# Performance work log

Hardware: AMD Instinct MI355X
Metric: run time of the kernel (lower is better)

Reference implementation:

```python
import jax, jax.numpy as jnp
import numpy as np
import math

HEADS = 8
DIM_HEAD = 64

def setup_inputs() -> dict:
    key = jax.random.key(0)
    ks = jax.random.split(key, 6)
    B, L, D = 2, 2048, 512
    Ls = 1936
    inner = HEADS * DIM_HEAD  # 512
    x = jax.random.normal(ks[0], (B, L, D), dtype=jnp.float32)
    positions = jax.random.normal(ks[1], (B, Ls, 2), dtype=jnp.float32) * 10.0
    w_qkv = jax.random.normal(ks[2], (3 * inner, D), dtype=jnp.float32) * (1.0 / math.sqrt(D))
    w_out = jax.random.normal(ks[3], (D, inner), dtype=jnp.float32) * (1.0 / math.sqrt(inner))
    b_out = jnp.zeros((D,), dtype=jnp.float32)
    log_sigma = jnp.full((HEADS,), math.log(3.0), dtype=jnp.float32)
    global_bias = jnp.float32(0.0)
    return {"x": x, "positions": positions, "w_qkv": w_qkv, "w_out": w_out,
            "b_out": b_out, "log_sigma": log_sigma, "global_bias": global_bias,
            "num_spatial": Ls}

def reference(x, positions, w_qkv, w_out, b_out, log_sigma, global_bias, num_spatial):
    B, L, D = x.shape
    H, Dh = HEADS, DIM_HEAD
    scale = Dh ** (-0.5)
    # qkv projection: [B,L,3*H*Dh] -> q,k,v each [B,H,L,Dh]
    qkv = jnp.einsum('bld,ed->ble', x, w_qkv)
    q, k, v = jnp.split(qkv, 3, axis=-1)
    def heads(t):
        return t.reshape(B, L, H, Dh).transpose(0, 2, 1, 3)
    q, k, v = heads(q), heads(k), heads(v)
    attn = jnp.einsum('bhid,bhjd->bhij', q, k) * scale  # [B,H,L,L]
    # Gaussian distance bias on the spatial block, global_bias elsewhere
    Ls = num_spatial
    diff = positions[:, :, None, :] - positions[:, None, :, :]  # [B,Ls,Ls,2]
    dist_sq = jnp.sum(diff * diff, axis=-1)                     # [B,Ls,Ls]
    sigma_sq = jnp.exp(log_sigma) ** 2                          # [H]
    spatial_bias = -dist_sq[:, None] / (2.0 * sigma_sq[None, :, None, None])  # [B,H,Ls,Ls]
    full_bias = jnp.full((B, H, L, L), global_bias, dtype=x.dtype)
    full_bias = full_bias.at[:, :, :Ls, :Ls].set(spatial_bias)
    attn = jax.nn.softmax(attn + full_bias, axis=-1)
    out = jnp.einsum('bhij,bhjd->bhid', attn, v)  # [B,H,L,Dh]
    out = out.transpose(0, 2, 1, 3).reshape(B, L, H * Dh)
    return jnp.einsum('ble,de->bld', out, w_out) + b_out
```

## Files before the change

kernel.cpp:

```cpp
#include <hip/hip_runtime.h>
#include <stdint.h>
#include <stddef.h>

#define NB   2
#define NL   2048
#define ND   512
#define NH   8
#define DH   64
#define LOG2E 1.44269504f
#define RG_TOT 32768
#define JS   4

typedef __attribute__((ext_vector_type(8))) short bf16x8;
typedef __attribute__((ext_vector_type(4))) float f32x4;

__device__ __forceinline__ unsigned short f2bf(float f) {
  union { float f; unsigned int u; } c; c.f = f;
  unsigned int u = c.u;
  unsigned int r = u + 0x7fffu + ((u >> 16) & 1u);
  return (unsigned short)(r >> 16);
}

__device__ __forceinline__ float bf2f(unsigned short u) {
  union { unsigned int i; float f; } c; c.i = ((unsigned int)u) << 16; return c.f;
}

__device__ __forceinline__ void split2(float v, unsigned short& h, unsigned short& l) {
  h = f2bf(v);
  l = f2bf(v - bf2f(h));
}

__device__ __forceinline__ float fexp2(float x) {
#if __has_builtin(__builtin_amdgcn_exp2f)
  return __builtin_amdgcn_exp2f(x);
#else
  return exp2f(x);
#endif
}

__device__ __forceinline__ void gl_lds16(const unsigned short* g, unsigned short* l) {
#if __has_builtin(__builtin_amdgcn_global_load_lds)
  __builtin_amdgcn_global_load_lds(
      (const __attribute__((address_space(1))) unsigned int*)g,
      (__attribute__((address_space(3))) unsigned int*)l, 16, 0, 0);
#else
  *(uint4*)l = *(const uint4*)g;
#endif
}

#define XC  524288
#define WQC 196608
#define WOC 65536
#define TOTC (XC + WQC + WOC)
__global__ void cvt_f32_bf16(const float* __restrict__ x, const float* __restrict__ wq,
                             const float* __restrict__ wo, const float* __restrict__ positions,
                             const int* __restrict__ ns_p,
                             unsigned short* __restrict__ xb, unsigned short* __restrict__ wqb,
                             unsigned short* __restrict__ wob, float* __restrict__ pospad) {
  int idx = blockIdx.x * 256 + threadIdx.x;
  if (idx < TOTC) {
    const float* src; unsigned short* dst; int off;
    if (idx < XC)            { src = x;  dst = xb;  off = idx; }
    else if (idx < XC + WQC) { src = wq; dst = wqb; off = idx - XC; }
    else                     { src = wo; dst = wob; off = idx - XC - WQC; }
    float4 f = ((const float4*)src)[off];
    ushort4 o;
    o.x = f2bf(f.x); o.y = f2bf(f.y); o.z = f2bf(f.z); o.w = f2bf(f.w);
    ((ushort4*)dst)[off] = o;
  } else {
    int i2 = idx - TOTC;
    if (i2 < NB * 1024) {
      int b = i2 >> 10;
      int jj = (i2 & 1023) * 2;
      int Ls = ns_p[0];
      float4 o = make_float4(0.f, 0.f, 0.f, 0.f);
      if (jj < Ls) { o.x = positions[((size_t)b * Ls + jj) * 2];
                     o.y = positions[((size_t)b * Ls + jj) * 2 + 1]; }
      if (jj + 1 < Ls) { o.z = positions[((size_t)b * Ls + jj + 1) * 2];
                         o.w = positions[((size_t)b * Ls + jj + 1) * 2 + 1]; }
      *(float4*)&pospad[((size_t)b * NL + jj) * 2] = o;
    }
  }
}

__global__ __launch_bounds__(256, 2) void gemm_qkv(
    const unsigned short* __restrict__ A, const unsigned short* __restrict__ Bm,
    unsigned short* __restrict__ qo, unsigned short* __restrict__ kp,
    unsigned short* __restrict__ vo)
{
  __shared__ __align__(16) unsigned short S[128 * 32 + 128 * 32];
  const int tid = threadIdx.x, wid = tid >> 6, lane = tid & 63;
  const int quad = lane >> 4, l15 = lane & 15;
  const int m0 = blockIdx.x * 128, n0 = blockIdx.y * 128;
  const int wm = (wid >> 1) * 64, wn = (wid & 1) * 64;

  f32x4 acc[4][4];
#pragma unroll
  for (int a = 0; a < 4; ++a)
#pragma unroll
    for (int b = 0; b < 4; ++b)
#pragma unroll
      for (int z = 0; z < 4; ++z) acc[a][b][z] = 0.f;

  for (int k0 = 0; k0 < ND; k0 += 32) {
#pragma unroll
    for (int p = 0; p < 4; ++p) {
      int c = p * 256 + wid * 64 + lane;
      if (c < 512) {
        int row = c >> 2, off = c & 3;
        gl_lds16(A + (size_t)(m0 + row) * ND + k0 + off * 8, &S[c * 8]);
      } else {
        int cb = c - 512;
        int row = cb >> 2, off = cb & 3;
        gl_lds16(Bm + (size_t)(n0 + row) * ND + k0 + off * 8, &S[c * 8]);
      }
    }
    __syncthreads();
    bf16x8 af[4], bfr[4];
#pragma unroll
    for (int mb = 0; mb < 4; ++mb)
      af[mb] = *(const bf16x8*)&S[(wm + mb * 16 + l15) * 32 + quad * 8];
#pragma unroll
    for (int nb = 0; nb < 4; ++nb)
      bfr[nb] = *(const bf16x8*)&S[4096 + (wn + nb * 16 + l15) * 32 + quad * 8];
#pragma unroll
    for (int mb = 0; mb < 4; ++mb)
#pragma unroll
      for (int nb = 0; nb < 4; ++nb)
        acc[mb][nb] = __builtin_amdgcn_mfma_f32_16x16x32_bf16(af[mb], bfr[nb], acc[mb][nb], 0, 0, 0);
    __syncthreads();
  }

  const float QSCALE = 0.125f * LOG2E;
#pragma unroll
  for (int mb = 0; mb < 4; ++mb) {
    int e0 = m0 + wm + mb * 16 + quad * 4;
    int s   = e0 >> 9;
    int hh  = (e0 >> 6) & 7;
    if (s == 1) {
      int kc  = mb >> 1;
      int q_t = ((mb & 1) << 1) + (quad >> 1);
      int par = quad & 1;
#pragma unroll
      for (int nb = 0; nb < 4; ++nb) {
        int token = n0 + wn + nb * 16 + l15;
        int bb = token >> 11, ll = token & 2047;
        int jt = ll >> 4;
        ushort4 o;
        o.x = f2bf(acc[mb][nb][0]);
        o.y = f2bf(acc[mb][nb][1]);
        o.z = f2bf(acc[mb][nb][2]);
        o.w = f2bf(acc[mb][nb][3]);
        size_t addr = (((size_t)(bb * NH + hh) * 128 + jt) * 2 + kc) * 512
                    + (q_t * 16 + l15) * 8 + par * 4;
        *(ushort4*)&kp[addr] = o;
      }
    } else {
      unsigned short* dst = (s == 0) ? qo : vo;
      float sc = (s == 0) ? QSCALE : 1.0f;
      int dh0 = e0 & 63;
#pragma unroll
      for (int nb = 0; nb < 4; ++nb) {
        int token = n0 + wn + nb * 16 + l15;
        int bb = token >> 11, ll = token & 2047;
        ushort4 o;
        o.x = f2bf(acc[mb][nb][0] * sc);
        o.y = f2bf(acc[mb][nb][1] * sc);
        o.z = f2bf(acc[mb][nb][2] * sc);
        o.w = f2bf(acc[mb][nb][3] * sc);
        *(ushort4*)&dst[(((size_t)bb * NH + hh) * NL + ll) * DH + dh0] = o;
      }
    }
  }
}

__global__ __launch_bounds__(256) void repack_v(
    const unsigned short* __restrict__ v, unsigned short* __restrict__ vp,
    const float* __restrict__ pospad, const float* __restrict__ log_sigma,
    const float* __restrict__ gbias_p, const int* __restrict__ ns_p,
    unsigned short* __restrict__ kext, unsigned short* __restrict__ qext)
{
  __shared__ unsigned short T[64][74];
  const int l0 = blockIdx.x * 64;
  const int bh = blockIdx.y;
  const int b  = bh >> 3, h = bh & 7;
  const int Ls = ns_p[0];
  const float gb  = gbias_p[0];
  const float sig = __expf(log_sigma[h]);
  const float CI  = LOG2E * 0.5f / (sig * sig);
  const float LGB = LOG2E * gb;
  const float* posb = pospad + (size_t)b * NL * 2;
  const int tid = threadIdx.x;

  const unsigned short* src = v + ((size_t)bh * NL + l0) * DH;
  unsigned short* dst = vp + (size_t)bh * 131072 + (size_t)(l0 >> 5) * 2048;
#pragma unroll
  for (int p = 0; p < 2; ++p) {
    int c = p * 256 + tid;
    int row = c >> 3, seg = c & 7;
    *(uint4*)&T[row][seg * 8] = *(const uint4*)(src + row * DH + seg * 8);
  }
  __syncthreads();
#pragma unroll
  for (int p = 0; p < 2; ++p) {
    int c = p * 256 + tid;
    int l15 = c & 15, q = (c >> 4) & 3, dht = (c >> 6) & 3, jcl = c >> 8;
    unsigned short u[8];
#pragma unroll
    for (int t = 0; t < 8; ++t) u[t] = T[jcl * 32 + q * 8 + t][dht * 16 + l15];
    *(uint4*)(dst + (size_t)jcl * 2048 + dht * 512 + (q * 16 + l15) * 8) = *(uint4*)u;
  }

  {
    int jtl  = tid >> 6;
    int lane = tid & 63;
    int quad = lane >> 4, l15 = lane & 15;
    int j = l0 + jtl * 16 + l15;
    unsigned short bv[16];
#pragma unroll
    for (int z = 0; z < 16; ++z) bv[z] = 0;
    if (j < Ls) {
      float2 p2 = *(const float2*)(posb + (size_t)j * 2);
      float rjC = -(CI * (p2.x * p2.x + p2.y * p2.y));
      unsigned short one = f2bf(1.0f);
      bv[0] = one; bv[1] = one;
      split2(rjC, bv[2], bv[3]);
      unsigned short Xh, Xl, Yh, Yl;
      split2(2.0f * CI * p2.x, Xh, Xl);
      split2(2.0f * CI * p2.y, Yh, Yl);
      bv[4] = Xh; bv[5] = Xh; bv[6] = Xl;
      bv[7] = Yh; bv[8] = Yh; bv[9] = Yl;
    }
    unsigned short o[8];
#pragma unroll
    for (int z = 0; z < 8; ++z) o[z] = bv[quad * 8 + z < 16 ? quad * 8 + z : 15];
    if (quad >= 2) {
#pragma unroll
      for (int z = 0; z < 8; ++z) o[z] = 0;
    }
    *(uint4*)(kext + ((size_t)bh * 128 + (l0 >> 4) + jtl) * 512 + lane * 8) = *(uint4*)o;
  }

  {
    int row = tid >> 2, seg = tid & 3;
    int i = l0 + row;
    unsigned short av[16];
#pragma unroll
    for (int z = 0; z < 16; ++z) av[z] = 0;
    if (i < Ls) {
      float2 p2 = *(const float2*)(posb + (size_t)i * 2);
      float riCm = -(CI * (p2.x * p2.x + p2.y * p2.y)) - LGB;
      unsigned short one = f2bf(1.0f);
      split2(riCm, av[0], av[1]);
      av[2] = one; av[3] = one;
      unsigned short xh, xl, yh, yl;
      split2(p2.x, xh, xl);
      split2(p2.y, yh, yl);
      av[4] = xh; av[5] = xl; av[6] = xh;
      av[7] = yh; av[8] = yl; av[9] = yh;
    }
    unsigned short o[8];
#pragma unroll
    for (int z = 0; z < 8; ++z) o[z] = (seg * 8 + z < 16) ? av[seg * 8 + z] : 0;
    if (seg >= 2) {
#pragma unroll
      for (int z = 0; z < 8; ++z) o[z] = 0;
    }
    *(uint4*)(qext + ((size_t)bh * NL + i) * 32 + seg * 8) = *(uint4*)o;
  }
}

__global__ __launch_bounds__(256, 2) void flash_kernel(
    const unsigned short* __restrict__ qb, const unsigned short* __restrict__ qeb,
    const unsigned short* __restrict__ kp, const unsigned short* __restrict__ keb,
    const unsigned short* __restrict__ vp, const float* __restrict__ gbias_p,
    unsigned short* __restrict__ Pb, float* __restrict__ rsbuf)
{
  const int it = blockIdx.x >> 2;
  const int js = blockIdx.x & 3;
  const int h  = blockIdx.y;
  const int b  = blockIdx.z;
  const int i0 = it * 128;
  const int jbase = js * (NL / JS);
  const float CBL = -8.0f * LOG2E + LOG2E * gbias_p[0];

  const int tid  = threadIdx.x;
  const int wid  = tid >> 6;
  const int lane = tid & 63;
  const int quad = lane >> 4;
  const int l15  = lane & 15;

  __shared__ __align__(16) unsigned short Ps[128][78];

  const size_t bh = (size_t)b * NH + h;
  const unsigned short* qbase  = qb  + (bh * NL + i0 + wid * 32) * DH;
  const unsigned short* qebase = qeb + (bh * NL + i0 + wid * 32) * 32;
  const unsigned short* kpb    = kp  + bh * 131072;
  const unsigned short* kebb   = keb + bh * 65536;
  const unsigned short* vpb    = vp  + bh * 131072;

  bf16x8 qf[2][2], qfe[2];
#pragma unroll
  for (int ib = 0; ib < 2; ++ib) {
#pragma unroll
    for (int kc = 0; kc < 2; ++kc)
      qf[ib][kc] = *(const bf16x8*)(qbase + (size_t)(ib * 16 + l15) * DH + kc * 32 + quad * 8);
    qfe[ib] = *(const bf16x8*)(qebase + (size_t)(ib * 16 + l15) * 32 + quad * 8);
  }

  f32x4 accO[4][2];
  float rsum[2];
#pragma unroll
  for (int d = 0; d < 4; ++d)
#pragma unroll
    for (int ib = 0; ib < 2; ++ib)
#pragma unroll
      for (int z = 0; z < 4; ++z) accO[d][ib][z] = 0.f;
  rsum[0] = 0.f; rsum[1] = 0.f;

  for (int jt = 0; jt < NL / JS / 64; ++jt) {
    const int j0 = jbase + jt * 64;
    const int jt0 = j0 >> 4;

    bf16x8 vf[4][2];
#pragma unroll
    for (int dht = 0; dht < 4; ++dht)
#pragma unroll
      for (int jc = 0; jc < 2; ++jc)
        vf[dht][jc] = *(const bf16x8*)(vpb + ((size_t)((j0 >> 5) + jc) * 4 + dht) * 512 + lane * 8);

#pragma unroll
    for (int jb = 0; jb < 4; ++jb) {
      bf16x8 kf0 = *(const bf16x8*)(kpb + ((size_t)(jt0 + jb) * 2 + 0) * 512 + lane * 8);
      bf16x8 kf1 = *(const bf16x8*)(kpb + ((size_t)(jt0 + jb) * 2 + 1) * 512 + lane * 8);
      bf16x8 kfe = *(const bf16x8*)(kebb + (size_t)(jt0 + jb) * 512 + lane * 8);
#pragma unroll
      for (int ib = 0; ib < 2; ++ib) {
        f32x4 accS;
#pragma unroll
        for (int z = 0; z < 4; ++z) accS[z] = 0.f;
        accS = __builtin_amdgcn_mfma_f32_16x16x32_bf16(kf0, qf[ib][0], accS, 0, 0, 0);
        accS = __builtin_amdgcn_mfma_f32_16x16x32_bf16(kf1, qf[ib][1], accS, 0, 0, 0);
        accS = __builtin_amdgcn_mfma_f32_16x16x32_bf16(kfe, qfe[ib], accS, 0, 0, 0);
        float p0 = fexp2(accS[0] + CBL);
        float p1 = fexp2(accS[1] + CBL);
        float p2 = fexp2(accS[2] + CBL);
        float p3 = fexp2(accS[3] + CBL);
        rsum[ib] += (p0 + p1) + (p2 + p3);
        uint2 w;
        w.x = (uint32_t)f2bf(p0) | ((uint32_t)f2bf(p1) << 16);
        w.y = (uint32_t)f2bf(p2) | ((uint32_t)f2bf(p3) << 16);
        *(uint2*)&Ps[wid * 32 + ib * 16 + l15][jb * 16 + quad * 4] = w;
      }
    }

    bf16x8 pf[2][2];
#pragma unroll
    for (int ib = 0; ib < 2; ++ib)
#pragma unroll
      for (int jc = 0; jc < 2; ++jc)
        pf[ib][jc] = *(const bf16x8*)&Ps[wid * 32 + ib * 16 + l15][jc * 32 + quad * 8];
#pragma unroll
    for (int dht = 0; dht < 4; ++dht)
#pragma unroll
      for (int ib = 0; ib < 2; ++ib) {
        accO[dht][ib] = __builtin_amdgcn_mfma_f32_16x16x32_bf16(vf[dht][0], pf[ib][0], accO[dht][ib], 0, 0, 0);
        accO[dht][ib] = __builtin_amdgcn_mfma_f32_16x16x32_bf16(vf[dht][1], pf[ib][1], accO[dht][ib], 0, 0, 0);
      }
  }

  const size_t rgbase = bh * NL + i0;
  const size_t poff = (size_t)js * RG_TOT * DH;
#pragma unroll
  for (int ib = 0; ib < 2; ++ib) {
    float v = rsum[ib];
    v += __shfl_xor(v, 16);
    v += __shfl_xor(v, 32);
    int irow = wid * 32 + ib * 16 + l15;
    if (quad == 0)
      rsbuf[(size_t)js * RG_TOT + rgbase + irow] = v;
#pragma unroll
    for (int dht = 0; dht < 4; ++dht) {
      ushort4 o;
      o.x = f2bf(accO[dht][ib][0]);
      o.y = f2bf(accO[dht][ib][1]);
      o.z = f2bf(accO[dht][ib][2]);
      o.w = f2bf(accO[dht][ib][3]);
      *(ushort4*)&Pb[poff + (rgbase + irow) * DH + dht * 16 + quad * 4] = o;
    }
  }
}

__global__ __launch_bounds__(256) void combine_kernel(const unsigned short* __restrict__ Pb,
                                                      const float* __restrict__ rsbuf,
                                                      unsigned short* __restrict__ attnb) {
  int idx = blockIdx.x * 256 + threadIdx.x;
  int rg = idx >> 4, c4 = idx & 15;
  float s0 = 0.f, s1 = 0.f, s2 = 0.f, s3 = 0.f, rsum = 0.f;
#pragma unroll
  for (int js = 0; js < JS; ++js) {
    ushort4 u = *(const ushort4*)&Pb[((size_t)js * RG_TOT + rg) * DH + c4 * 4];
    s0 += bf2f(u.x); s1 += bf2f(u.y); s2 += bf2f(u.z); s3 += bf2f(u.w);
    rsum += rsbuf[(size_t)js * RG_TOT + rg];
  }
  float rs = 1.0f / rsum;
  int bhm = rg >> 11;
  int l   = rg & 2047;
  int bb  = bhm >> 3, hh = bhm & 7;
  ushort4 o;
  o.x = f2bf(s0 * rs);
  o.y = f2bf(s1 * rs);
  o.z = f2bf(s2 * rs);
  o.w = f2bf(s3 * rs);
  *(ushort4*)&attnb[(((size_t)bb * NL + l) * ND) + hh * DH + c4 * 4] = o;
}

__global__ __launch_bounds__(256, 2) void gemm_out(
    const unsigned short* __restrict__ A, const unsigned short* __restrict__ Bm,
    const float* __restrict__ bias, float* __restrict__ out)
{
  __shared__ __align__(16) unsigned short S[64 * 32 + 128 * 32];
  const int tid = threadIdx.x, wid = tid >> 6, lane = tid & 63;
  const int quad = lane >> 4, l15 = lane & 15;
  const int m0 = blockIdx.x * 64, n0 = blockIdx.y * 128;
  const int wm = (wid >> 1) * 32, wn = (wid & 1) * 64;

  f32x4 acc[2][4];
#pragma unroll
  for (int a = 0; a < 2; ++a)
#pragma unroll
    for (int b = 0; b < 4; ++b)
#pragma unroll
      for (int z = 0; z < 4; ++z) acc[a][b][z] = 0.f;

  for (int k0 = 0; k0 < ND; k0 += 32) {
#pragma unroll
    for (int p = 0; p < 3; ++p) {
      int c = p * 256 + wid * 64 + lane;
      if (c < 256) {
        int row = c >> 2, off = c & 3;
        gl_lds16(A + (size_t)(m0 + row) * ND + k0 + off * 8, &S[c * 8]);
      } else {
        int cb = c - 256;
        int row = cb >> 2, off = cb & 3;
        gl_lds16(Bm + (size_t)(n0 + row) * ND + k0 + off * 8, &S[2048 + cb * 8]);
      }
    }
    __syncthreads();
    bf16x8 af[2], bfr[4];
#pragma unroll
    for (int mb = 0; mb < 2; ++mb)
      af[mb] = *(const bf16x8*)&S[(wm + mb * 16 + l15) * 32 + quad * 8];
#pragma unroll
    for (int nb = 0; nb < 4; ++nb)
      bfr[nb] = *(const bf16x8*)&S[2048 + (wn + nb * 16 + l15) * 32 + quad * 8];
#pragma unroll
    for (int mb = 0; mb < 2; ++mb)
#pragma unroll
      for (int nb = 0; nb < 4; ++nb)
        acc[mb][nb] = __builtin_amdgcn_mfma_f32_16x16x32_bf16(af[mb], bfr[nb], acc[mb][nb], 0, 0, 0);
    __syncthreads();
  }

#pragma unroll
  for (int mb = 0; mb < 2; ++mb) {
    int e0 = m0 + wm + mb * 16 + quad * 4;
    float4 bv = *(const float4*)&bias[e0];
#pragma unroll
    for (int nb = 0; nb < 4; ++nb) {
      int token = n0 + wn + nb * 16 + l15;
      float4 o;
      o.x = acc[mb][nb][0] + bv.x;
      o.y = acc[mb][nb][1] + bv.y;
      o.z = acc[mb][nb][2] + bv.z;
      o.w = acc[mb][nb][3] + bv.w;
      *(float4*)&out[(size_t)token * ND + e0] = o;
    }
  }
}

extern "C" void kernel_launch(void* const* d_in, const int* in_sizes, int n_in,
                              void* d_out, int out_size, void* d_ws, size_t ws_size,
                              hipStream_t stream) {
  const float* x         = (const float*)d_in[0];
  const float* positions = (const float*)d_in[1];
  const float* w_qkv     = (const float*)d_in[2];
  const float* w_out     = (const float*)d_in[3];
  const float* b_out     = (const float*)d_in[4];
  const float* log_sigma = (const float*)d_in[5];
  const float* gbias     = (const float*)d_in[6];
  const int*   ns        = (const int*)d_in[7];

  unsigned short* ws   = (unsigned short*)d_ws;
  unsigned short* xb   = ws;
  unsigned short* wob  = xb   + 2097152;
  unsigned short* qbf  = wob  + 262144;
  unsigned short* kpf  = qbf  + 2097152;
  unsigned short* vbf  = kpf  + 2097152;
  unsigned short* vpf  = vbf  + 2097152;
  unsigned short* qext = vpf  + 2097152;
  unsigned short* kext = qext + 1048576;
  float* pospad = (float*)(kext + 1048576);
  unsigned short* R    = (unsigned short*)(pospad + NB * NL * 2);
  unsigned short* wqb  = R;
  unsigned short* Pb   = R;
  float* rsbuf = (float*)(Pb + (size_t)JS * RG_TOT * DH);

  cvt_f32_bf16<<<(TOTC + NB * 1024 + 255) / 256, 256, 0, stream>>>(
      x, w_qkv, w_out, positions, ns, xb, wqb, wob, pospad);

  dim3 g1((3 * NH * DH) / 128, NB * NL / 128);
  gemm_qkv<<<g1, 256, 0, stream>>>(wqb, xb, qbf, kpf, vbf);

  dim3 gr(NL / 64, NB * NH);
  repack_v<<<gr, 256, 0, stream>>>(vbf, vpf, pospad, log_sigma, gbias, ns, kext, qext);

  dim3 g2((NL / 128) * JS, NH, NB);
  flash_kernel<<<g2, 256, 0, stream>>>(qbf, qext, kpf, kext, vpf, gbias, Pb, rsbuf);

  combine_kernel<<<RG_TOT * 16 / 256, 256, 0, stream>>>(Pb, rsbuf, xb);

  dim3 g3(ND / 64, NB * NL / 128);
  gemm_out<<<g3, 256, 0, stream>>>(wob, xb, b_out, (float*)d_out);
}
```

Before: 152.8 us.

## Fuse V repack into QKV GEMM epilogue and extension build into convert kernel

Drops the separate repack_v kernel. The QKV GEMM epilogue now writes V directly in the packed MFMA-friendly layout, and the convert kernel builds the q/k positional extension vectors straight from positions, so the pospad buffer is no longer needed. This removes one launch, a full V round trip through memory, and an LDS transpose. The cost is scattered 2-byte stores in the GEMM epilogue for V. The flash kernel's launch bounds also rise to 3 blocks per SM, which may force register spills.

Result: faster. 146.6 us (-4.0%).

```diff
diff --git a/kernel.cpp b/kernel.cpp
--- a/kernel.cpp
+++ b/kernel.cpp
@@ -52,11 +52,13 @@
 #define WQC 196608
 #define WOC 65536
 #define TOTC (XC + WQC + WOC)
-__global__ void cvt_f32_bf16(const float* __restrict__ x, const float* __restrict__ wq,
-                             const float* __restrict__ wo, const float* __restrict__ positions,
-                             const int* __restrict__ ns_p,
-                             unsigned short* __restrict__ xb, unsigned short* __restrict__ wqb,
-                             unsigned short* __restrict__ wob, float* __restrict__ pospad) {
+__global__ void cvt_ext(const float* __restrict__ x, const float* __restrict__ wq,
+                        const float* __restrict__ wo, const float* __restrict__ positions,
+                        const float* __restrict__ log_sigma, const float* __restrict__ gbias_p,
+                        const int* __restrict__ ns_p,
+                        unsigned short* __restrict__ xb, unsigned short* __restrict__ wqb,
+                        unsigned short* __restrict__ wob,
+                        unsigned short* __restrict__ kext, unsigned short* __restrict__ qext) {
   int idx = blockIdx.x * 256 + threadIdx.x;
   if (idx < TOTC) {
     const float* src; unsigned short* dst; int off;
@@ -67,26 +69,68 @@
     ushort4 o;
     o.x = f2bf(f.x); o.y = f2bf(f.y); o.z = f2bf(f.z); o.w = f2bf(f.w);
     ((ushort4*)dst)[off] = o;
+    return;
+  }
+  int t2 = idx - TOTC;
+  int bh = (t2 >> 11) & 15;
+  int j  = t2 & 2047;
+  int b  = bh >> 3, h = bh & 7;
+  int Ls = ns_p[0];
+  float sig = __expf(log_sigma[h]);
+  float CI  = LOG2E * 0.5f / (sig * sig);
+  uint4 z = make_uint4(0u, 0u, 0u, 0u);
+  if (t2 < 32768) {
+    unsigned short bv[16];
+#pragma unroll
+    for (int q = 0; q < 16; ++q) bv[q] = 0;
+    if (j < Ls) {
+      float px = positions[((size_t)b * Ls + j) * 2];
+      float py = positions[((size_t)b * Ls + j) * 2 + 1];
+      float rjC = -(CI * (px * px + py * py));
+      unsigned short one = f2bf(1.0f);
+      bv[0] = one; bv[1] = one;
+      split2(rjC, bv[2], bv[3]);
+      unsigned short Xh, Xl, Yh, Yl;
+      split2(2.0f * CI * px, Xh, Xl);
+      split2(2.0f * CI * py, Yh, Yl);
+      bv[4] = Xh; bv[5] = Xh; bv[6] = Xl;
+      bv[7] = Yh; bv[8] = Yh; bv[9] = Yl;
+    }
+    unsigned short* kx = kext + ((size_t)bh * 128 + (j >> 4)) * 512 + (size_t)(j & 15) * 8;
+    *(uint4*)(kx)       = *(uint4*)&bv[0];
+    *(uint4*)(kx + 128) = *(uint4*)&bv[8];
+    *(uint4*)(kx + 256) = z;
+    *(uint4*)(kx + 384) = z;
   } else {
-    int i2 = idx - TOTC;
-    if (i2 < NB * 1024) {
-      int b = i2 >> 10;
-      int jj = (i2 & 1023) * 2;
-      int Ls = ns_p[0];
-      float4 o = make_float4(0.f, 0.f, 0.f, 0.f);
-      if (jj < Ls) { o.x = positions[((size_t)b * Ls + jj) * 2];
-                     o.y = positions[((size_t)b * Ls + jj) * 2 + 1]; }
-      if (jj + 1 < Ls) { o.z = positions[((size_t)b * Ls + jj + 1) * 2];
-                         o.w = positions[((size_t)b * Ls + jj + 1) * 2 + 1]; }
-      *(float4*)&pospad[((size_t)b * NL + jj) * 2] = o;
-    }
+    unsigned short av[16];
+#pragma unroll
+    for (int q = 0; q < 16; ++q) av[q] = 0;
+    if (j < Ls) {
+      float px = positions[((size_t)b * Ls + j) * 2];
+      float py = positions[((size_t)b * Ls + j) * 2 + 1];
+      float LGB = LOG2E * gbias_p[0];
+      float riCm = -(CI * (px * px + py * py)) - LGB;
+      unsigned short one = f2bf(1.0f);
+      split2(riCm, av[0], av[1]);
+      av[2] = one; av[3] = one;
+      unsigned short xh, xl, yh, yl;
+      split2(px, xh, xl);
+      split2(py, yh, yl);
+      av[4] = xh; av[5] = xl; av[6] = xh;
+      av[7] = yh; av[8] = yl; av[9] = yh;
+    }
+    unsigned short* qx = qext + ((size_t)bh * NL + j) * 32;
+    *(uint4*)(qx)      = *(uint4*)&av[0];
+    *(uint4*)(qx + 8)  = *(uint4*)&av[8];
+    *(uint4*)(qx + 16) = z;
+    *(uint4*)(qx + 24) = z;
   }
 }
 
 __global__ __launch_bounds__(256, 2) void gemm_qkv(
     const unsigned short* __restrict__ A, const unsigned short* __restrict__ Bm,
     unsigned short* __restrict__ qo, unsigned short* __restrict__ kp,
-    unsigned short* __restrict__ vo)
+    unsigned short* __restrict__ vp)
 {
   __shared__ __align__(16) unsigned short S[128 * 32 + 128 * 32];
   const int tid = threadIdx.x, wid = tid >> 6, lane = tid & 63;
@@ -155,122 +199,38 @@
                     + (q_t * 16 + l15) * 8 + par * 4;
         *(ushort4*)&kp[addr] = o;
       }
+    } else if (s == 2) {
+      int dh0 = e0 & 63;
+      int dht = dh0 >> 4;
+      int dl  = dh0 & 15;
+#pragma unroll
+      for (int nb = 0; nb < 4; ++nb) {
+        int token = n0 + wn + nb * 16 + l15;
+        int bb = token >> 11, ll = token & 2047;
+        size_t base = (((size_t)(bb * NH + hh) * 64 + (ll >> 5)) * 4 + dht) * 512
+                    + (size_t)(((ll >> 3) & 3)) * 128 + (ll & 7);
+#pragma unroll
+        for (int r = 0; r < 4; ++r)
+          vp[base + (size_t)(dl + r) * 8] = f2bf(acc[mb][nb][r]);
+      }
     } else {
-      unsigned short* dst = (s == 0) ? qo : vo;
-      float sc = (s == 0) ? QSCALE : 1.0f;
       int dh0 = e0 & 63;
 #pragma unroll
       for (int nb = 0; nb < 4; ++nb) {
         int token = n0 + wn + nb * 16 + l15;
         int bb = token >> 11, ll = token & 2047;
         ushort4 o;
-        o.x = f2bf(acc[mb][nb][0] * sc);
-        o.y = f2bf(acc[mb][nb][1] * sc);
-        o.z = f2bf(acc[mb][nb][2] * sc);
-        o.w = f2bf(acc[mb][nb][3] * sc);
-        *(ushort4*)&dst[(((size_t)bb * NH + hh) * NL + ll) * DH + dh0] = o;
-      }
-    }
-  }
-}
-
-__global__ __launch_bounds__(256) void repack_v(
-    const unsigned short* __restrict__ v, unsigned short* __restrict__ vp,
-    const float* __restrict__ pospad, const float* __restrict__ log_sigma,
-    const float* __restrict__ gbias_p, const int* __restrict__ ns_p,
-    unsigned short* __restrict__ kext, unsigned short* __restrict__ qext)
-{
-  __shared__ unsigned short T[64][74];
-  const int l0 = blockIdx.x * 64;
-  const int bh = blockIdx.y;
-  const int b  = bh >> 3, h = bh & 7;
-  const int Ls = ns_p[0];
-  const float gb  = gbias_p[0];
-  const float sig = __expf(log_sigma[h]);
-  const float CI  = LOG2E * 0.5f / (sig * sig);
-  const float LGB = LOG2E * gb;
-  const float* posb = pospad + (size_t)b * NL * 2;
-  const int tid = threadIdx.x;
-
-  const unsigned short* src = v + ((size_t)bh * NL + l0) * DH;
-  unsigned short* dst = vp + (size_t)bh * 131072 + (size_t)(l0 >> 5) * 2048;
-#pragma unroll
-  for (int p = 0; p < 2; ++p) {
-    int c = p * 256 + tid;
-    int row = c >> 3, seg = c & 7;
-    *(uint4*)&T[row][seg * 8] = *(const uint4*)(src + row * DH + seg * 8);
-  }
-  __syncthreads();
-#pragma unroll
-  for (int p = 0; p < 2; ++p) {
-    int c = p * 256 + tid;
-    int l15 = c & 15, q = (c >> 4) & 3, dht = (c >> 6) & 3, jcl = c >> 8;
-    unsigned short u[8];
-#pragma unroll
-    for (int t = 0; t < 8; ++t) u[t] = T[jcl * 32 + q * 8 + t][dht * 16 + l15];
-    *(uint4*)(dst + (size_t)jcl * 2048 + dht * 512 + (q * 16 + l15) * 8) = *(uint4*)u;
-  }
-
-  {
-    int jtl  = tid >> 6;
-    int lane = tid & 63;
-    int quad = lane >> 4, l15 = lane & 15;
-    int j = l0 + jtl * 16 + l15;
-    unsigned short bv[16];
-#pragma unroll
-    for (int z = 0; z < 16; ++z) bv[z] = 0;
-    if (j < Ls) {
-      float2 p2 = *(const float2*)(posb + (size_t)j * 2);
-      float rjC = -(CI * (p2.x * p2.x + p2.y * p2.y));
-      unsigned short one = f2bf(1.0f);
-      bv[0] = one; bv[1] = one;
-      split2(rjC, bv[2], bv[3]);
-      unsigned short Xh, Xl, Yh, Yl;
-      split2(2.0f * CI * p2.x, Xh, Xl);
-      split2(2.0f * CI * p2.y, Yh, Yl);
-      bv[4] = Xh; bv[5] = Xh; bv[6] = Xl;
-      bv[7] = Yh; bv[8] = Yh; bv[9] = Yl;
-    }
-    unsigned short o[8];
-#pragma unroll
-    for (int z = 0; z < 8; ++z) o[z] = bv[quad * 8 + z < 16 ? quad * 8 + z : 15];
-    if (quad >= 2) {
-#pragma unroll
-      for (int z = 0; z < 8; ++z) o[z] = 0;
-    }
-    *(uint4*)(kext + ((size_t)bh * 128 + (l0 >> 4) + jtl) * 512 + lane * 8) = *(uint4*)o;
-  }
-
-  {
-    int row = tid >> 2, seg = tid & 3;
-    int i = l0 + row;
-    unsigned short av[16];
-#pragma unroll
-    for (int z = 0; z < 16; ++z) av[z] = 0;
-    if (i < Ls) {
-      float2 p2 = *(const float2*)(posb + (size_t)i * 2);
-      float riCm = -(CI * (p2.x * p2.x + p2.y * p2.y)) - LGB;
-      unsigned short one = f2bf(1.0f);
-      split2(riCm, av[0], av[1]);
-      av[2] = one; av[3] = one;
-      unsigned short xh, xl, yh, yl;
-      split2(p2.x, xh, xl);
-      split2(p2.y, yh, yl);
-      av[4] = xh; av[5] = xl; av[6] = xh;
-      av[7] = yh; av[8] = yl; av[9] = yh;
-    }
-    unsigned short o[8];
-#pragma unroll
-    for (int z = 0; z < 8; ++z) o[z] = (seg * 8 + z < 16) ? av[seg * 8 + z] : 0;
-    if (seg >= 2) {
-#pragma unroll
-      for (int z = 0; z < 8; ++z) o[z] = 0;
-    }
-    *(uint4*)(qext + ((size_t)bh * NL + i) * 32 + seg * 8) = *(uint4*)o;
-  }
-}
-
-__global__ __launch_bounds__(256, 2) void flash_kernel(
+        o.x = f2bf(acc[mb][nb][0] * QSCALE);
+        o.y = f2bf(acc[mb][nb][1] * QSCALE);
+        o.z = f2bf(acc[mb][nb][2] * QSCALE);
+        o.w = f2bf(acc[mb][nb][3] * QSCALE);
+        *(ushort4*)&qo[(((size_t)bb * NH + hh) * NL + ll) * DH + dh0] = o;
+      }
+    }
+  }
+}
+
+__global__ __launch_bounds__(256, 3) void flash_kernel(
     const unsigned short* __restrict__ qb, const unsigned short* __restrict__ qeb,
     const unsigned short* __restrict__ kp, const unsigned short* __restrict__ keb,
     const unsigned short* __restrict__ vp, const float* __restrict__ gbias_p,
@@ -496,24 +456,19 @@
   unsigned short* wob  = xb   + 2097152;
   unsigned short* qbf  = wob  + 262144;
   unsigned short* kpf  = qbf  + 2097152;
-  unsigned short* vbf  = kpf  + 2097152;
-  unsigned short* vpf  = vbf  + 2097152;
+  unsigned short* vpf  = kpf  + 2097152;
   unsigned short* qext = vpf  + 2097152;
   unsigned short* kext = qext + 1048576;
-  float* pospad = (float*)(kext + 1048576);
-  unsigned short* R    = (unsigned short*)(pospad + NB * NL * 2);
+  unsigned short* R    = kext + 1048576;
   unsigned short* wqb  = R;
   unsigned short* Pb   = R;
   float* rsbuf = (float*)(Pb + (size_t)JS * RG_TOT * DH);
 
-  cvt_f32_bf16<<<(TOTC + NB * 1024 + 255) / 256, 256, 0, stream>>>(
-      x, w_qkv, w_out, positions, ns, xb, wqb, wob, pospad);
+  cvt_ext<<<(TOTC + 65536) / 256, 256, 0, stream>>>(
+      x, w_qkv, w_out, positions, log_sigma, gbias, ns, xb, wqb, wob, kext, qext);
 
   dim3 g1((3 * NH * DH) / 128, NB * NL / 128);
-  gemm_qkv<<<g1, 256, 0, stream>>>(wqb, xb, qbf, kpf, vbf);
-
-  dim3 gr(NL / 64, NB * NH);
-  repack_v<<<gr, 256, 0, stream>>>(vbf, vpf, pospad, log_sigma, gbias, ns, kext, qext);
+  gemm_qkv<<<g1, 256, 0, stream>>>(wqb, xb, qbf, kpf, vpf);
 
   dim3 g2((NL / 128) * JS, NH, NB);
   flash_kernel<<<g2, 256, 0, stream>>>(qbf, qext, kpf, kext, vpf, gbias, Pb, rsbuf);
```
